# Performance work log

Measured on AMD Instinct MI355X. Metric: run time of the kernel, lower is better.

The kernel has to match this reference:

```python
import jax, jax.numpy as jnp
import numpy as np

B, HO, WO = 16, 1024, 1024
W = H = 2048


def setup_inputs() -> dict:
    key = jax.random.key(0)
    ks = jax.random.split(key, 5)
    inp = {"x": jax.random.uniform(ks[0], (B, HO, WO, 2), dtype=jnp.float32)}
    for i, d in enumerate([1, 2, 4, 8]):
        # torch shape (1,1,W//d,H//d): dim2 is sampled-H, dim3 is sampled-W
        inp[f"layer{i+1}"] = jax.random.normal(ks[i + 1], (1, 1, W // d, H // d), dtype=jnp.float32) * 0.1
    return inp


def _grid_sample_1ch(tex, grid):
    """Bilinear grid_sample, zeros padding, align_corners=False (torch default).
    tex: [Hi, Wi] single-channel texture shared across batch.
    grid: [B, Ho, Wo, 2] in [-1, 1], last dim = (x, y).
    returns [B, Ho, Wo].
    """
    Hi, Wi = tex.shape
    ix = ((grid[..., 0] + 1.0) * Wi - 1.0) * 0.5
    iy = ((grid[..., 1] + 1.0) * Hi - 1.0) * 0.5
    x0f = jnp.floor(ix)
    y0f = jnp.floor(iy)
    wx1 = ix - x0f
    wy1 = iy - y0f
    wx0 = 1.0 - wx1
    wy0 = 1.0 - wy1
    x0 = x0f.astype(jnp.int32)
    y0 = y0f.astype(jnp.int32)
    x1 = x0 + 1
    y1 = y0 + 1

    def fetch(yy, xx):
        valid = (yy >= 0) & (yy < Hi) & (xx >= 0) & (xx < Wi)
        yc = jnp.clip(yy, 0, Hi - 1)
        xc = jnp.clip(xx, 0, Wi - 1)
        return jnp.where(valid, tex[yc, xc], 0.0)

    return (fetch(y0, x0) * wy0 * wx0 + fetch(y0, x1) * wy0 * wx1
            + fetch(y1, x0) * wy1 * wx0 + fetch(y1, x1) * wy1 * wx1)


def reference(x, layer1, layer2, layer3, layer4):
    grid = x * 2.0 - 1.0  # [B, Ho, Wo, 2]
    y = (_grid_sample_1ch(layer1[0, 0], grid)
         + _grid_sample_1ch(layer2[0, 0], grid)
         + _grid_sample_1ch(layer3[0, 0], grid)
         + _grid_sample_1ch(layer4[0, 0], grid))
    return y[:, None, :, :]  # [B, 1, Ho, Wo] to match torch output
```

## Files before the change

### kernel.cpp

```cpp
#include <hip/hip_runtime.h>

typedef float vf4 __attribute__((ext_vector_type(4)));
typedef float vf2 __attribute__((ext_vector_type(2)));
typedef _Float16 h4 __attribute__((ext_vector_type(4)));


__device__ __forceinline__ vf2 fetch_pair(const float* __restrict__ tex, int N, int y, int x0) {
    vf2 r = {0.f, 0.f};
    if ((unsigned)y < (unsigned)N) {
        const float* row = tex + (size_t)(unsigned)y * (unsigned)N;
        if ((unsigned)x0 < (unsigned)(N - 1)) {
            __builtin_memcpy(&r, row + x0, sizeof(vf2));
        } else if (x0 == -1) {
            r.y = row[0];
        } else if (x0 == N - 1) {
            r.x = row[N - 1];
        }
    }
    return r;
}

__device__ __forceinline__ float sample_ix(const float* __restrict__ tex, int N, float ix, float iy) {
    float x0f = floorf(ix);
    float y0f = floorf(iy);
    float wx = ix - x0f;
    float wy = iy - y0f;
    int x0 = (int)x0f;
    int y0 = (int)y0f;
    vf2 t = fetch_pair(tex, N, y0, x0);
    vf2 b = fetch_pair(tex, N, y0 + 1, x0);
    float top = fmaf(wx, t.y - t.x, t.x);
    float bot = fmaf(wx, b.y - b.x, b.x);
    return fmaf(wy, bot - top, top);
}

__device__ __forceinline__ float knotV(const float* __restrict__ l1, const float* __restrict__ l2,
                                       const float* __restrict__ l3, const float* __restrict__ l4,
                                       float fx, float fy) {
    float s;
    s  = sample_ix(l1, 2048, fmaf(fx, 0.5f,    -0.5f), fmaf(fy, 0.5f,    -0.5f));
    s += sample_ix(l2, 1024, fmaf(fx, 0.25f,   -0.5f), fmaf(fy, 0.25f,   -0.5f));
    s += sample_ix(l3,  512, fmaf(fx, 0.125f,  -0.5f), fmaf(fy, 0.125f,  -0.5f));
    s += sample_ix(l4,  256, fmaf(fx, 0.0625f, -0.5f), fmaf(fy, 0.0625f, -0.5f));
    return s;
}

__global__ void __launch_bounds__(256) build_R_tiled(
    const float* __restrict__ l1, const float* __restrict__ l2,
    const float* __restrict__ l3, const float* __restrict__ l4,
    h4* __restrict__ R) {
    __shared__ float Vs[65][66];
    const int tx = (blockIdx.x & 63) << 6;
    const int ty = (blockIdx.x >> 6) << 6;
    for (int k = threadIdx.x; k < 65 * 65; k += 256) {
        int ky = k / 65;
        int kx = k - ky * 65;
        Vs[ky][kx] = knotV(l1, l2, l3, l4, (float)(tx + kx), (float)(ty + ky));
    }
    __syncthreads();
    #pragma unroll
    for (int i = 0; i < 16; ++i) {
        int c = (i << 8) + threadIdx.x;
        int cy = c >> 6;
        int cx = c & 63;
        h4 q = { (_Float16)Vs[cy][cx],     (_Float16)Vs[cy][cx + 1],
                 (_Float16)Vs[cy + 1][cx], (_Float16)Vs[cy + 1][cx + 1] };
        R[(size_t)(ty + cy) * 4096 + (tx + cx)] = q;
    }
}

__device__ __forceinline__ float sample_R(const h4* __restrict__ R, float gx, float gy) {
    float u = gx * 4096.0f;
    float v = gy * 4096.0f;
    int jx = min((int)u, 4095);
    int jy = min((int)v, 4095);
    float wx = u - (float)jx;
    float wy = v - (float)jy;
    h4 q = R[((size_t)jy << 12) | (unsigned)jx];
    float v00 = (float)q.x, v01 = (float)q.y, v10 = (float)q.z, v11 = (float)q.w;
    float top = fmaf(wx, v01 - v00, v00);
    float bot = fmaf(wx, v11 - v10, v10);
    return fmaf(wy, bot - top, top);
}

__global__ void __launch_bounds__(256) tex_kernel_fused(
    const vf4* __restrict__ xg, const h4* __restrict__ R,
    vf4* __restrict__ out, int nquads) {
    int t = blockIdx.x * blockDim.x + threadIdx.x;
    if (t >= nquads) return;
    vf4 a = __builtin_nontemporal_load(&xg[2 * t]);
    vf4 b = __builtin_nontemporal_load(&xg[2 * t + 1]);
    vf4 o;
    o.x = sample_R(R, a.x, a.y);
    o.y = sample_R(R, a.z, a.w);
    o.z = sample_R(R, b.x, b.y);
    o.w = sample_R(R, b.z, b.w);
    __builtin_nontemporal_store(o, &out[t]);
}

__device__ __forceinline__ float sample1(const float* __restrict__ tex, int N, float gx, float gy) {
    return sample_ix(tex, N, fmaf(gx, (float)N, -0.5f), fmaf(gy, (float)N, -0.5f));
}

__global__ void __launch_bounds__(256) tex_kernel_direct(
    const vf4* __restrict__ xg,
    const float* __restrict__ l1, const float* __restrict__ l2,
    const float* __restrict__ l3, const float* __restrict__ l4,
    vf4* __restrict__ out, int nquads) {
    int t = blockIdx.x * blockDim.x + threadIdx.x;
    if (t >= nquads) return;
    vf4 a = __builtin_nontemporal_load(&xg[2 * t]);
    vf4 b = __builtin_nontemporal_load(&xg[2 * t + 1]);
    vf4 o;
    o.x = sample1(l1, 2048, a.x, a.y) + sample1(l2, 1024, a.x, a.y) + sample1(l3, 512, a.x, a.y) + sample1(l4, 256, a.x, a.y);
    o.y = sample1(l1, 2048, a.z, a.w) + sample1(l2, 1024, a.z, a.w) + sample1(l3, 512, a.z, a.w) + sample1(l4, 256, a.z, a.w);
    o.z = sample1(l1, 2048, b.x, b.y) + sample1(l2, 1024, b.x, b.y) + sample1(l3, 512, b.x, b.y) + sample1(l4, 256, b.x, b.y);
    o.w = sample1(l1, 2048, b.z, b.w) + sample1(l2, 1024, b.z, b.w) + sample1(l3, 512, b.z, b.w) + sample1(l4, 256, b.z, b.w);
    __builtin_nontemporal_store(o, &out[t]);
}

extern "C" void kernel_launch(void* const* d_in, const int* in_sizes, int n_in,
                              void* d_out, int out_size, void* d_ws, size_t ws_size,
                              hipStream_t stream) {
    const vf4* xg = (const vf4*)d_in[0];
    const float* l1 = (const float*)d_in[1];
    const float* l2 = (const float*)d_in[2];
    const float* l3 = (const float*)d_in[3];
    const float* l4 = (const float*)d_in[4];
    vf4* out = (vf4*)d_out;
    int nquads = out_size / 4;
    const size_t R_bytes = (size_t)4096 * 4096 * 8;

    if (ws_size >= R_bytes) {
        h4* R = (h4*)d_ws;
        build_R_tiled<<<4096, 256, 0, stream>>>(l1, l2, l3, l4, R);
        tex_kernel_fused<<<(nquads + 255) / 256, 256, 0, stream>>>(xg, R, out, nquads);
    } else {
        tex_kernel_direct<<<(nquads + 255) / 256, 256, 0, stream>>>(xg, l1, l2, l3, l4, out, nquads);
    }
}
```

Before: 470.9 us.

## Build lookup table with separable bilinear interpolation via shared-memory row pass

The table-building kernel now interpolates horizontally first, computing each needed texture row once per tile into a shared-memory buffer (68 rows across the four levels). It then does the vertical interpolation per knot from that buffer. Before, every knot issued four 2D bilinear samples straight to global memory. This removes redundant global fetches and repeated x-weight math, at the cost of an extra shared buffer, a second barrier and lower occupancy. The main sampling kernel is unchanged, so the gain is limited to the build phase.

```diff
diff --git a/kernel.cpp b/kernel.cpp
--- a/kernel.cpp
+++ b/kernel.cpp
@@ -34,30 +34,57 @@
     return fmaf(wy, bot - top, top);
 }
 
-__device__ __forceinline__ float knotV(const float* __restrict__ l1, const float* __restrict__ l2,
-                                       const float* __restrict__ l3, const float* __restrict__ l4,
-                                       float fx, float fy) {
-    float s;
-    s  = sample_ix(l1, 2048, fmaf(fx, 0.5f,    -0.5f), fmaf(fy, 0.5f,    -0.5f));
-    s += sample_ix(l2, 1024, fmaf(fx, 0.25f,   -0.5f), fmaf(fy, 0.25f,   -0.5f));
-    s += sample_ix(l3,  512, fmaf(fx, 0.125f,  -0.5f), fmaf(fy, 0.125f,  -0.5f));
-    s += sample_ix(l4,  256, fmaf(fx, 0.0625f, -0.5f), fmaf(fy, 0.0625f, -0.5f));
-    return s;
-}
-
-__global__ void __launch_bounds__(256) build_R_tiled(
+__global__ void __launch_bounds__(256) build_R_sep(
     const float* __restrict__ l1, const float* __restrict__ l2,
     const float* __restrict__ l3, const float* __restrict__ l4,
     h4* __restrict__ R) {
+    __shared__ float H[68][66];
     __shared__ float Vs[65][66];
     const int tx = (blockIdx.x & 63) << 6;
     const int ty = (blockIdx.x >> 6) << 6;
+
+    for (int w = threadIdx.x; w < 68 * 65; w += 256) {
+        int slot = w / 65;
+        int kx = w - slot * 65;
+        const float* tex;
+        int N, bs, ry0;
+        float cc;
+        if (slot < 34)      { tex = l1; N = 2048; cc = 0.5f;    bs = 0;  ry0 = (ty >> 1) - 1; }
+        else if (slot < 52) { tex = l2; N = 1024; cc = 0.25f;   bs = 34; ry0 = (ty >> 2) - 1; }
+        else if (slot < 62) { tex = l3; N = 512;  cc = 0.125f;  bs = 52; ry0 = (ty >> 3) - 1; }
+        else                { tex = l4; N = 256;  cc = 0.0625f; bs = 62; ry0 = (ty >> 4) - 1; }
+        int ry = ry0 + (slot - bs);
+        float ix = fmaf((float)(tx + kx), cc, -0.5f);
+        float x0f = floorf(ix);
+        float wx = ix - x0f;
+        vf2 p = fetch_pair(tex, N, ry, (int)x0f);
+        H[slot][kx] = fmaf(wx, p.y - p.x, p.x);
+    }
+    __syncthreads();
+
     for (int k = threadIdx.x; k < 65 * 65; k += 256) {
         int ky = k / 65;
         int kx = k - ky * 65;
-        Vs[ky][kx] = knotV(l1, l2, l3, l4, (float)(tx + kx), (float)(ty + ky));
+        float jy = (float)(ty + ky);
+        float s = 0.f;
+        #pragma unroll
+        for (int l = 0; l < 4; ++l) {
+            const float cc = (l == 0) ? 0.5f : (l == 1) ? 0.25f : (l == 2) ? 0.125f : 0.0625f;
+            const int bs   = (l == 0) ? 0    : (l == 1) ? 34    : (l == 2) ? 52     : 62;
+            const int ry0  = (l == 0) ? ((ty >> 1) - 1) : (l == 1) ? ((ty >> 2) - 1)
+                           : (l == 2) ? ((ty >> 3) - 1) : ((ty >> 4) - 1);
+            float iy = fmaf(jy, cc, -0.5f);
+            float y0f = floorf(iy);
+            float wy = iy - y0f;
+            int slot = bs + ((int)y0f - ry0);
+            float a = H[slot][kx];
+            float b = H[slot + 1][kx];
+            s += fmaf(wy, b - a, a);
+        }
+        Vs[ky][kx] = s;
     }
     __syncthreads();
+
     #pragma unroll
     for (int i = 0; i < 16; ++i) {
         int c = (i << 8) + threadIdx.x;
@@ -133,7 +160,7 @@
 
     if (ws_size >= R_bytes) {
         h4* R = (h4*)d_ws;
-        build_R_tiled<<<4096, 256, 0, stream>>>(l1, l2, l3, l4, R);
+        build_R_sep<<<4096, 256, 0, stream>>>(l1, l2, l3, l4, R);
         tex_kernel_fused<<<(nquads + 255) / 256, 256, 0, stream>>>(xg, R, out, nquads);
     } else {
         tex_kernel_direct<<<(nquads + 255) / 256, 256, 0, stream>>>(xg, l1, l2, l3, l4, out, nquads);
```

Measured after the change: 400.5 us. -14.9%, faster.
